# Optimization experiments

Measured on AMD Instinct MI355X. Metric: run time of the kernel, lower is better.

## Reference

```python
import jax, jax.numpy as jnp
import numpy as np

H = 16       # num_attention_heads
HKV = 4      # num_key_value_heads
HD = 128     # head_dim
G = H // HKV # num_key_value_groups


def setup_inputs() -> dict:
    key = jax.random.key(0)
    ks = jax.random.split(key, 7)
    s = 0.02
    B, S, D = 2, 2048, 2048
    return {
        "hidden_states": jax.random.normal(ks[0], (B, S, D), jnp.float32),
        "Wq": jax.random.normal(ks[1], (D, H * HD), jnp.float32) * s,
        "Wk": jax.random.normal(ks[2], (D, HKV * HD), jnp.float32) * s,
        "Wv": jax.random.normal(ks[3], (D, HKV * HD), jnp.float32) * s,
        "Wg": jax.random.normal(ks[4], (H * HD, HKV), jnp.float32) * s,
        "Wd": jax.random.normal(ks[5], (HKV * HD, HKV), jnp.float32) * s,
        "Wo": jax.random.normal(ks[6], (H * HD, D), jnp.float32) * s,
    }


def reference(hidden_states, Wq, Wk, Wv, Wg, Wd, Wo):
    b, s, _ = hidden_states.shape
    scale = HD ** -0.5

    q_flat = hidden_states @ Wq                    # [b,s,H*HD]
    k_flat = hidden_states @ Wk                    # [b,s,HKV*HD]
    v_flat = hidden_states @ Wv                    # [b,s,HKV*HD]

    gate = q_flat @ Wg                             # [b,s,HKV] (per query pos)
    delta = v_flat @ Wd                            # [b,s,HKV] (per key pos)
    # attn_bias: [b,HKV,key_len] after transpose; broadcast over query dim
    bias = (jax.nn.sigmoid(gate) * delta).transpose(0, 2, 1)  # [b,HKV,s]

    # [b,HKV,G,s,HD] query grouped by kv-head; [b,HKV,s,HD] key/value
    q = q_flat.reshape(b, s, HKV, G, HD).transpose(0, 2, 3, 1, 4)
    k = k_flat.reshape(b, s, HKV, HD).transpose(0, 2, 1, 3)
    v = v_flat.reshape(b, s, HKV, HD).transpose(0, 2, 1, 3)

    scores = jnp.einsum('bngqd,bnkd->bngqk', q, k) * scale  # [b,HKV,G,s,s]
    logits = scores + bias[:, :, None, None, :]

    causal = jnp.tril(jnp.ones((s, s), dtype=bool))
    # 'relu' mask: key positions allowed only where relu(bias) > 0
    allowed = causal[None, None, None] & (bias > 0)[:, :, None, None, :]
    neg = jnp.finfo(logits.dtype).min
    logits = jnp.where(allowed, logits, neg)

    p = jax.nn.softmax(logits, axis=-1)
    o = jnp.einsum('bngqk,bnkd->bngqd', p, v)               # [b,HKV,G,s,HD]
    o = o.transpose(0, 3, 1, 2, 4).reshape(b, s, H * HD)
    return o @ Wo
```

## Files before the change

### kernel.cpp

```cpp
#include <hip/hip_runtime.h>
#include <hip/hip_bf16.h>
#include <cmath>
#include <cstdint>

typedef __attribute__((ext_vector_type(8))) short short8;
typedef __attribute__((ext_vector_type(4))) float floatx4;
typedef __attribute__((ext_vector_type(4))) unsigned int uintx4;

typedef const __attribute__((address_space(1))) unsigned int* gas_p;
typedef __attribute__((address_space(3))) unsigned int* las_p;

#define LOG2E 1.4426950408889634f

__device__ inline unsigned short f2bf(float f) {
  unsigned int u = __builtin_bit_cast(unsigned int, f);
  unsigned int r = (u + 0x7FFFu + ((u >> 16) & 1u)) >> 16;
  return (unsigned short)r;
}
__device__ inline float bf2f(unsigned short h) {
  unsigned int u = ((unsigned int)h) << 16;
  return __builtin_bit_cast(float, u);
}

__global__ void k_f32_to_bf16(const float* __restrict__ in, unsigned short* __restrict__ out, int n4) {
  int i = blockIdx.x * 256 + threadIdx.x;
  if (i >= n4) return;
  float4 v = reinterpret_cast<const float4*>(in)[i];
  uint2 o;
  o.x = (unsigned)f2bf(v.x) | ((unsigned)f2bf(v.y) << 16);
  o.y = (unsigned)f2bf(v.z) | ((unsigned)f2bf(v.w) << 16);
  reinterpret_cast<uint2*>(out)[i] = o;
}

__global__ void k_transpose_w(const float* __restrict__ in, unsigned short* __restrict__ out,
                              int K, int N, float scl) {
  __shared__ float t[32][33];
  int n0 = blockIdx.x * 32, k0 = blockIdx.y * 32;
  int tx = threadIdx.x & 31, ty = threadIdx.x >> 5;
  #pragma unroll
  for (int r = ty; r < 32; r += 8)
    t[r][tx] = in[(long)(k0 + r) * N + n0 + tx];
  __syncthreads();
  #pragma unroll
  for (int r = ty; r < 32; r += 8)
    out[(long)(n0 + r) * K + k0 + tx] = f2bf(t[tx][r] * scl);
}

__global__ void k_wproj(const float* __restrict__ W, const float* __restrict__ Ws,
                        float* __restrict__ out, int Kw) {
  int d = blockIdx.x;
  float a0 = 0, a1 = 0, a2 = 0, a3 = 0;
  for (int j = threadIdx.x; j < Kw; j += 256) {
    float w = W[(long)d * Kw + j];
    float4 g = reinterpret_cast<const float4*>(Ws)[j];
    a0 += w * g.x; a1 += w * g.y; a2 += w * g.z; a3 += w * g.w;
  }
  #pragma unroll
  for (int off = 1; off < 64; off <<= 1) {
    a0 += __shfl_xor(a0, off, 64); a1 += __shfl_xor(a1, off, 64);
    a2 += __shfl_xor(a2, off, 64); a3 += __shfl_xor(a3, off, 64);
  }
  __shared__ float red[4][4];
  if ((threadIdx.x & 63) == 0) {
    int wv = threadIdx.x >> 6;
    red[wv][0] = a0; red[wv][1] = a1; red[wv][2] = a2; red[wv][3] = a3;
  }
  __syncthreads();
  if (threadIdx.x < 4) {
    int nn = threadIdx.x;
    out[d * 4 + nn] = red[0][nn] + red[1][nn] + red[2][nn] + red[3][nn];
  }
}

__global__ void k_bias(const float* __restrict__ hs, const float* __restrict__ Wqg,
                       const float* __restrict__ Wvd, float* __restrict__ bias) {
  int row = blockIdx.x;
  int b = row >> 11, s = row & 2047;
  float g0 = 0, g1 = 0, g2 = 0, g3 = 0, d0 = 0, d1 = 0, d2 = 0, d3 = 0;
  const float* h = hs + (long)row * 2048;
  for (int j = threadIdx.x; j < 2048; j += 256) {
    float x = h[j];
    float4 a = reinterpret_cast<const float4*>(Wqg)[j];
    float4 c = reinterpret_cast<const float4*>(Wvd)[j];
    g0 += x * a.x; g1 += x * a.y; g2 += x * a.z; g3 += x * a.w;
    d0 += x * c.x; d1 += x * c.y; d2 += x * c.z; d3 += x * c.w;
  }
  #pragma unroll
  for (int off = 1; off < 64; off <<= 1) {
    g0 += __shfl_xor(g0, off, 64); g1 += __shfl_xor(g1, off, 64);
    g2 += __shfl_xor(g2, off, 64); g3 += __shfl_xor(g3, off, 64);
    d0 += __shfl_xor(d0, off, 64); d1 += __shfl_xor(d1, off, 64);
    d2 += __shfl_xor(d2, off, 64); d3 += __shfl_xor(d3, off, 64);
  }
  __shared__ float red[4][8];
  if ((threadIdx.x & 63) == 0) {
    int wv = threadIdx.x >> 6;
    red[wv][0] = g0; red[wv][1] = g1; red[wv][2] = g2; red[wv][3] = g3;
    red[wv][4] = d0; red[wv][5] = d1; red[wv][6] = d2; red[wv][7] = d3;
  }
  __syncthreads();
  if (threadIdx.x < 4) {
    int nn = threadIdx.x;
    float gg = red[0][nn] + red[1][nn] + red[2][nn] + red[3][nn];
    float dd = red[0][4 + nn] + red[1][4 + nn] + red[2][4 + nn] + red[3][4 + nn];
    float sig = 1.0f / (1.0f + __expf(-gg));
    float v = sig * dd;
    bias[(b * 4 + nn) * 2048 + s] = (v > 0.0f) ? v * LOG2E : -INFINITY;
  }
}

template <int WRITE_BF16>
__global__ __launch_bounds__(256, 2) void k_gemm_bt(
    const unsigned short* __restrict__ A, const unsigned short* __restrict__ Bt,
    void* __restrict__ Cout, int M, int N, int K) {
  __shared__ __align__(16) unsigned short As[128 * 32];
  __shared__ __align__(16) unsigned short Bs[128 * 32];
  const int tid = threadIdx.x;
  const int lane = tid & 63, wave = tid >> 6;
  const int quad = lane >> 4, l16 = lane & 15;
  const long bm = (long)blockIdx.y * 128, bn = (long)blockIdx.x * 128;
  const int wm = (wave >> 1) * 64, wn = (wave & 1) * 64;

  const floatx4 fz = {0.f, 0.f, 0.f, 0.f};
  floatx4 acc[4][4];
  #pragma unroll
  for (int i = 0; i < 4; i++)
    #pragma unroll
    for (int j = 0; j < 4; j++) acc[i][j] = fz;

  const int r0 = tid >> 2, c0 = (tid & 3) * 8;
  const unsigned short* Ag = A + (bm + r0) * K + c0;
  const unsigned short* Bg = Bt + (bn + r0) * K + c0;
  unsigned short* AsW0 = As + (wave * 16) * 32;
  unsigned short* AsW1 = As + (wave * 16 + 64) * 32;
  unsigned short* BsW0 = Bs + (wave * 16) * 32;
  unsigned short* BsW1 = Bs + (wave * 16 + 64) * 32;

  for (int kt = 0; kt < K; kt += 32) {
    __syncthreads();
    __builtin_amdgcn_global_load_lds((gas_p)(const void*)(Ag + kt),
                                     (las_p)(void*)AsW0, 16, 0, 0);
    __builtin_amdgcn_global_load_lds((gas_p)(const void*)(Ag + (long)64 * K + kt),
                                     (las_p)(void*)AsW1, 16, 0, 0);
    __builtin_amdgcn_global_load_lds((gas_p)(const void*)(Bg + kt),
                                     (las_p)(void*)BsW0, 16, 0, 0);
    __builtin_amdgcn_global_load_lds((gas_p)(const void*)(Bg + (long)64 * K + kt),
                                     (las_p)(void*)BsW1, 16, 0, 0);
    __syncthreads();
    short8 af[4], bf[4];
    #pragma unroll
    for (int i = 0; i < 4; i++)
      af[i] = *reinterpret_cast<const short8*>(&As[(wm + i * 16 + l16) * 32 + quad * 8]);
    #pragma unroll
    for (int j = 0; j < 4; j++)
      bf[j] = *reinterpret_cast<const short8*>(&Bs[(wn + j * 16 + l16) * 32 + quad * 8]);
    #pragma unroll
    for (int i = 0; i < 4; i++)
      #pragma unroll
      for (int j = 0; j < 4; j++)
        acc[i][j] = __builtin_amdgcn_mfma_f32_16x16x32_bf16(af[i], bf[j], acc[i][j], 0, 0, 0);
  }
  #pragma unroll
  for (int i = 0; i < 4; i++)
    #pragma unroll
    for (int j = 0; j < 4; j++)
      #pragma unroll
      for (int r = 0; r < 4; r++) {
        const long row = bm + wm + i * 16 + quad * 4 + r;
        const long col = bn + wn + j * 16 + l16;
        const float v = acc[i][j][r];
        if (WRITE_BF16)
          ((unsigned short*)Cout)[row * N + col] = f2bf(v);
        else
          ((float*)Cout)[row * N + col] = v;
      }
}

__global__ void k_transpose_v(const unsigned short* __restrict__ qkv, unsigned short* __restrict__ vt) {
  __shared__ unsigned short t[32][33];
  int c0 = blockIdx.x * 32, s0 = blockIdx.y * 32, b = blockIdx.z;
  int tx = threadIdx.x & 31, ty = threadIdx.x >> 5;
  #pragma unroll
  for (int r = ty; r < 32; r += 8)
    t[r][tx] = qkv[((long)(b * 2048 + s0 + r)) * 3072 + 2560 + c0 + tx];
  __syncthreads();
  #pragma unroll
  for (int r = ty; r < 32; r += 8)
    vt[((long)(b * 512 + c0 + r)) * 2048 + s0 + tx] = t[tx][r];
}

__global__ void k_vmean2(const unsigned short* __restrict__ vT, float* __restrict__ vmean) {
  const int row = blockIdx.x;
  const int tid = threadIdx.x, lane = tid & 63, wave = tid >> 6;
  uintx4 v = reinterpret_cast<const uintx4*>(vT + (long)row * 2048)[tid];
  float s = 0.f;
  #pragma unroll
  for (int i = 0; i < 4; i++) {
    unsigned u = v[i];
    s += bf2f((unsigned short)(u & 0xffff)) + bf2f((unsigned short)(u >> 16));
  }
  #pragma unroll
  for (int off = 1; off < 64; off <<= 1) s += __shfl_xor(s, off, 64);
  __shared__ float red[4];
  if (lane == 0) red[wave] = s;
  __syncthreads();
  if (tid == 0) vmean[row] = (red[0] + red[1] + red[2] + red[3]) * (1.0f / 2048.0f);
}

__global__ __launch_bounds__(256, 3) void k_attn(
    const unsigned short* __restrict__ qkv,
    const float* __restrict__ biasb,
    const unsigned short* __restrict__ vT,
    const float* __restrict__ vmean,
    unsigned short* __restrict__ o)
{
  int idx = blockIdx.x;
  const int g = idx & 3;
  const int n = (idx >> 2) & 3;
  const int b = (idx >> 4) & 1;
  const int qt = 31 - (idx >> 5);
  const int tid = threadIdx.x, lane = tid & 63, wave = tid >> 6;
  const int quad = lane >> 4, l16 = lane & 15;
  const int q0 = qt * 64 + wave * 16;

  __shared__ __align__(16) unsigned short Ks[64 * 144];
  __shared__ __align__(16) unsigned short Vs[128 * 72];
  __shared__ __align__(16) unsigned short Ps[4 * 16 * 72];
  unsigned short* Psw = Ps + wave * 1152;

  short8 qf[4];
  {
    const unsigned short* qp = qkv + (long)(b * 2048) * 3072 + (n * 4 + g) * 128;
    #pragma unroll
    for (int ks = 0; ks < 4; ks++)
      qf[ks] = *reinterpret_cast<const short8*>(
          qp + (long)(q0 + l16) * 3072 + ks * 32 + quad * 8);
  }

  const floatx4 fz = {0.f, 0.f, 0.f, 0.f};
  floatx4 oacc[8];
  #pragma unroll
  for (int j = 0; j < 8; j++) oacc[j] = fz;
  float mrow = -INFINITY, lrow = 0.0f;

  const float* biasrow = biasb + (b * 4 + n) * 2048;
  const unsigned short* kbase = qkv + (long)(b * 2048) * 3072 + 2048 + n * 128;
  const unsigned short* vbase = vT + (long)(b * 512 + n * 128) * 2048;
  const int kk_ = tid >> 4, hdo_ = (tid & 15) * 8;
  const int hd_ = tid >> 3, ko_ = (tid & 7) * 8;

  uintx4 kreg[4], vreg[4];
  float4 breg[4];
  {
    const unsigned short* kp = kbase;
    const unsigned short* vp = vbase;
    #pragma unroll
    for (int it = 0; it < 4; it++)
      kreg[it] = *reinterpret_cast<const uintx4*>(kp + (long)(kk_ + it * 16) * 3072 + hdo_);
    #pragma unroll
    for (int it = 0; it < 4; it++)
      vreg[it] = *reinterpret_cast<const uintx4*>(vp + (long)(hd_ + it * 32) * 2048 + ko_);
    #pragma unroll
    for (int kt = 0; kt < 4; kt++)
      breg[kt] = *reinterpret_cast<const float4*>(biasrow + kt * 16 + quad * 4);
  }

  const int kend = qt * 64 + 64;
  for (int k0 = 0; k0 < kend; k0 += 64) {
    __syncthreads();
    #pragma unroll
    for (int it = 0; it < 4; it++)
      *reinterpret_cast<uintx4*>(&Ks[(kk_ + it * 16) * 144 + hdo_]) = kreg[it];
    #pragma unroll
    for (int it = 0; it < 4; it++)
      *reinterpret_cast<uintx4*>(&Vs[(hd_ + it * 32) * 72 + ko_]) = vreg[it];
    float4 bcur[4];
    #pragma unroll
    for (int kt = 0; kt < 4; kt++) bcur[kt] = breg[kt];

    if (k0 + 64 < kend) {
      const unsigned short* kp = kbase + (long)(k0 + 64) * 3072;
      const unsigned short* vp = vbase + (k0 + 64);
      #pragma unroll
      for (int it = 0; it < 4; it++)
        kreg[it] = *reinterpret_cast<const uintx4*>(kp + (long)(kk_ + it * 16) * 3072 + hdo_);
      #pragma unroll
      for (int it = 0; it < 4; it++)
        vreg[it] = *reinterpret_cast<const uintx4*>(vp + (long)(hd_ + it * 32) * 2048 + ko_);
      #pragma unroll
      for (int kt = 0; kt < 4; kt++)
        breg[kt] = *reinterpret_cast<const float4*>(biasrow + (k0 + 64) + kt * 16 + quad * 4);
    }
    __syncthreads();

    const bool active = (k0 <= q0 + 15);
    if (active) {
      floatx4 sacc[4];
      #pragma unroll
      for (int kt = 0; kt < 4; kt++)
        sacc[kt] = (floatx4){bcur[kt].x, bcur[kt].y, bcur[kt].z, bcur[kt].w};
      #pragma unroll
      for (int ks = 0; ks < 4; ks++) {
        short8 kf[4];
        #pragma unroll
        for (int kt = 0; kt < 4; kt++)
          kf[kt] = *reinterpret_cast<const short8*>(&Ks[(kt * 16 + l16) * 144 + ks * 32 + quad * 8]);
        #pragma unroll
        for (int kt = 0; kt < 4; kt++)
          sacc[kt] = __builtin_amdgcn_mfma_f32_16x16x32_bf16(kf[kt], qf[ks], sacc[kt], 0, 0, 0);
      }

      const bool full = (k0 + 63 <= q0);
      if (!full) {
        const int diff = (q0 + l16) - (k0 + quad * 4);
        #pragma unroll
        for (int kt = 0; kt < 4; kt++)
          #pragma unroll
          for (int r = 0; r < 4; r++)
            if (kt * 16 + r > diff) sacc[kt][r] = -INFINITY;
      }
      float mx = -INFINITY;
      #pragma unroll
      for (int kt = 0; kt < 4; kt++)
        #pragma unroll
        for (int r = 0; r < 4; r++) mx = fmaxf(mx, sacc[kt][r]);
      mx = fmaxf(mx, __shfl_xor(mx, 16, 64));
      mx = fmaxf(mx, __shfl_xor(mx, 32, 64));
      const float mn = fmaxf(mrow, mx);
      const float mnc = fmaxf(mn, -1e38f);
      const float alpha = __builtin_amdgcn_exp2f(mrow - mnc);
      float rs = 0.0f;
      unsigned pk[4][2];
      #pragma unroll
      for (int kt = 0; kt < 4; kt++) {
        #pragma unroll
        for (int r = 0; r < 4; r++) {
          float p = __builtin_amdgcn_exp2f(sacc[kt][r] - mnc);
          sacc[kt][r] = p;
          rs += p;
        }
        #pragma unroll
        for (int r2 = 0; r2 < 2; r2++)
          pk[kt][r2] = (unsigned)f2bf(sacc[kt][2 * r2]) | ((unsigned)f2bf(sacc[kt][2 * r2 + 1]) << 16);
      }
      rs += __shfl_xor(rs, 16, 64);
      rs += __shfl_xor(rs, 32, 64);
      mrow = mn;
      lrow = lrow * alpha + rs;

      float al[4];
      #pragma unroll
      for (int r = 0; r < 4; r++) al[r] = __shfl(alpha, quad * 4 + r, 64);
      #pragma unroll
      for (int j = 0; j < 8; j++)
        #pragma unroll
        for (int r = 0; r < 4; r++) oacc[j][r] *= al[r];

      unsigned* Pd = reinterpret_cast<unsigned*>(Psw);
      #pragma unroll
      for (int kt = 0; kt < 4; kt++)
        #pragma unroll
        for (int r2 = 0; r2 < 2; r2++)
          Pd[l16 * 36 + kt * 8 + quad * 2 + r2] = pk[kt][r2];

      #pragma unroll
      for (int ks2 = 0; ks2 < 2; ks2++) {
        short8 pf = *reinterpret_cast<const short8*>(&Psw[l16 * 72 + ks2 * 32 + quad * 8]);
        #pragma unroll
        for (int j = 0; j < 8; j++) {
          short8 vf = *reinterpret_cast<const short8*>(&Vs[(j * 16 + l16) * 72 + ks2 * 32 + quad * 8]);
          oacc[j] = __builtin_amdgcn_mfma_f32_16x16x32_bf16(pf, vf, oacc[j], 0, 0, 0);
        }
      }
    }
  }

  const long obase = (long)(b * 2048) * 2048 + (n * 4 + g) * 128;
  #pragma unroll
  for (int r = 0; r < 4; r++) {
    const int qrow = q0 + quad * 4 + r;
    const float l = __shfl(lrow, quad * 4 + r, 64);
    const float inv = (l > 0.0f) ? 1.0f / l : 0.0f;
    #pragma unroll
    for (int j = 0; j < 8; j++) {
      const int hd = j * 16 + l16;
      float v = oacc[j][r] * inv;
      if (l <= 0.0f) v = vmean[(b * 4 + n) * 128 + hd];
      o[obase + (long)qrow * 2048 + hd] = f2bf(v);
    }
  }
}

extern "C" void kernel_launch(void* const* d_in, const int* in_sizes, int n_in,
                              void* d_out, int out_size, void* d_ws, size_t ws_size,
                              hipStream_t stream) {
  const float* hs = (const float*)d_in[0];
  const float* Wq = (const float*)d_in[1];
  const float* Wk = (const float*)d_in[2];
  const float* Wv = (const float*)d_in[3];
  const float* Wg = (const float*)d_in[4];
  const float* Wd = (const float*)d_in[5];
  const float* Wo = (const float*)d_in[6];
  float* out = (float*)d_out;

  char* ws = (char*)d_ws;
  unsigned short* hsb   = (unsigned short*)(ws);
  unsigned short* Wcomb = (unsigned short*)(ws + 16777216);
  unsigned short* Wot   = (unsigned short*)(ws + 29360128);
  float*  Wqg   = (float*)(ws + 37748736);
  float*  Wvd   = (float*)(ws + 37781504);
  float*  biasb = (float*)(ws + 37814272);
  unsigned short* qkv = (unsigned short*)(ws + 37879808);
  unsigned short* vT  = (unsigned short*)(ws + 63045632);
  float*  vmean = (float*)(ws + 67239936);
  unsigned short* ob  = (unsigned short*)(ws + 67244032);

  const float QSCALE = 0.08838834764831845f * LOG2E;

  k_f32_to_bf16<<<2097152 / 256, 256, 0, stream>>>(hs, hsb, 2097152);

  {
    dim3 g1(2048 / 32, 2048 / 32);
    dim3 g2(512 / 32, 2048 / 32);
    k_transpose_w<<<g1, 256, 0, stream>>>(Wq, Wcomb, 2048, 2048, QSCALE);
    k_transpose_w<<<g2, 256, 0, stream>>>(Wk, Wcomb + (long)2048 * 2048, 2048, 512, 1.0f);
    k_transpose_w<<<g2, 256, 0, stream>>>(Wv, Wcomb + (long)2560 * 2048, 2048, 512, 1.0f);
    k_transpose_w<<<g1, 256, 0, stream>>>(Wo, Wot, 2048, 2048, 1.0f);
  }

  k_wproj<<<2048, 256, 0, stream>>>(Wq, Wg, Wqg, 2048);
  k_wproj<<<2048, 256, 0, stream>>>(Wv, Wd, Wvd, 512);

  k_bias<<<4096, 256, 0, stream>>>(hs, Wqg, Wvd, biasb);

  {
    dim3 gq(3072 / 128, 4096 / 128);
    k_gemm_bt<1><<<gq, 256, 0, stream>>>(hsb, Wcomb, qkv, 4096, 3072, 2048);
  }

  {
    dim3 gv(16, 64, 2);
    k_transpose_v<<<gv, 256, 0, stream>>>(qkv, vT);
  }

  k_vmean2<<<1024, 256, 0, stream>>>(vT, vmean);

  k_attn<<<1024, 256, 0, stream>>>(qkv, biasb, vT, vmean, ob);

  {
    dim3 go(2048 / 128, 4096 / 128);
    k_gemm_bt<0><<<go, 256, 0, stream>>>(ob, Wot, out, 4096, 2048, 2048);
  }
}
```

Before: 348.4 us.

## Swizzle LDS tiles, lazy softmax rescale, interleave tile order, raise occupancy

Replaces padded LDS layouts for K, V and P with XOR-swizzled unpadded layouts. This cuts shared memory use and lets launch bounds ask for 4 blocks per CU instead of 3. It reorders query tiles across the grid to balance causal work, and skips the output rescale when the running max grows by no more than 8 (in log2 units). It also adds s_setprio around the MFMA sections and uses the hardware packed bf16 convert instruction. The lazy rescale may risk overflow or precision loss, and the swizzle must match between writes and reads.

```diff
diff --git a/kernel.cpp b/kernel.cpp
--- a/kernel.cpp
+++ b/kernel.cpp
@@ -207,7 +207,7 @@
   if (tid == 0) vmean[row] = (red[0] + red[1] + red[2] + red[3]) * (1.0f / 2048.0f);
 }
 
-__global__ __launch_bounds__(256, 3) void k_attn(
+__global__ __launch_bounds__(256, 4) void k_attn(
     const unsigned short* __restrict__ qkv,
     const float* __restrict__ biasb,
     const unsigned short* __restrict__ vT,
@@ -218,15 +218,22 @@
   const int g = idx & 3;
   const int n = (idx >> 2) & 3;
   const int b = (idx >> 4) & 1;
-  const int qt = 31 - (idx >> 5);
+  const int i5 = idx >> 5, pj = i5 & 7, phi = i5 >> 3;
+  int qt;
+  if (phi == 0) qt = 31 - pj;
+  else if (phi == 1) qt = pj;
+  else if (phi == 2) qt = 23 - pj;
+  else qt = 8 + pj;
+
   const int tid = threadIdx.x, lane = tid & 63, wave = tid >> 6;
   const int quad = lane >> 4, l16 = lane & 15;
   const int q0 = qt * 64 + wave * 16;
 
-  __shared__ __align__(16) unsigned short Ks[64 * 144];
-  __shared__ __align__(16) unsigned short Vs[128 * 72];
-  __shared__ __align__(16) unsigned short Ps[4 * 16 * 72];
-  unsigned short* Psw = Ps + wave * 1152;
+  __shared__ __align__(16) unsigned short Ks[64 * 128];
+  __shared__ __align__(16) unsigned short Vs[128 * 64];
+  __shared__ __align__(16) unsigned short Ps[4 * 16 * 64];
+  unsigned short* Psw = Ps + wave * 1024;
+  const int swz = (l16 & 7) << 3;
 
   short8 qf[4];
   {
@@ -248,6 +255,8 @@
   const unsigned short* vbase = vT + (long)(b * 512 + n * 128) * 2048;
   const int kk_ = tid >> 4, hdo_ = (tid & 15) * 8;
   const int hd_ = tid >> 3, ko_ = (tid & 7) * 8;
+  const int kswz = (kk_ & 7) << 3;
+  const int vswz = (hd_ & 7) << 3;
 
   uintx4 kreg[4], vreg[4];
   float4 breg[4];
@@ -270,10 +279,10 @@
     __syncthreads();
     #pragma unroll
     for (int it = 0; it < 4; it++)
-      *reinterpret_cast<uintx4*>(&Ks[(kk_ + it * 16) * 144 + hdo_]) = kreg[it];
+      *reinterpret_cast<uintx4*>(&Ks[(kk_ + it * 16) * 128 + (hdo_ ^ kswz)]) = kreg[it];
     #pragma unroll
     for (int it = 0; it < 4; it++)
-      *reinterpret_cast<uintx4*>(&Vs[(hd_ + it * 32) * 72 + ko_]) = vreg[it];
+      *reinterpret_cast<uintx4*>(&Vs[(hd_ + it * 32) * 64 + (ko_ ^ vswz)]) = vreg[it];
     float4 bcur[4];
     #pragma unroll
     for (int kt = 0; kt < 4; kt++) bcur[kt] = breg[kt];
@@ -299,16 +308,19 @@
       #pragma unroll
       for (int kt = 0; kt < 4; kt++)
         sacc[kt] = (floatx4){bcur[kt].x, bcur[kt].y, bcur[kt].z, bcur[kt].w};
+      __builtin_amdgcn_s_setprio(1);
       #pragma unroll
       for (int ks = 0; ks < 4; ks++) {
         short8 kf[4];
         #pragma unroll
         for (int kt = 0; kt < 4; kt++)
-          kf[kt] = *reinterpret_cast<const short8*>(&Ks[(kt * 16 + l16) * 144 + ks * 32 + quad * 8]);
+          kf[kt] = *reinterpret_cast<const short8*>(
+              &Ks[(kt * 16 + l16) * 128 + ((ks * 32 + quad * 8) ^ swz)]);
         #pragma unroll
         for (int kt = 0; kt < 4; kt++)
           sacc[kt] = __builtin_amdgcn_mfma_f32_16x16x32_bf16(kf[kt], qf[ks], sacc[kt], 0, 0, 0);
       }
+      __builtin_amdgcn_s_setprio(0);
 
       const bool full = (k0 + 63 <= q0);
       if (!full) {
@@ -326,9 +338,21 @@
         for (int r = 0; r < 4; r++) mx = fmaxf(mx, sacc[kt][r]);
       mx = fmaxf(mx, __shfl_xor(mx, 16, 64));
       mx = fmaxf(mx, __shfl_xor(mx, 32, 64));
-      const float mn = fmaxf(mrow, mx);
-      const float mnc = fmaxf(mn, -1e38f);
-      const float alpha = __builtin_amdgcn_exp2f(mrow - mnc);
+      if (!__all(mx <= mrow + 8.0f)) {
+        const float mn = fmaxf(mrow, mx);
+        const float mnc2 = fmaxf(mn, -1e38f);
+        const float alpha = __builtin_amdgcn_exp2f(mrow - mnc2);
+        float al[4];
+        #pragma unroll
+        for (int r = 0; r < 4; r++) al[r] = __shfl(alpha, quad * 4 + r, 64);
+        #pragma unroll
+        for (int j = 0; j < 8; j++)
+          #pragma unroll
+          for (int r = 0; r < 4; r++) oacc[j][r] *= al[r];
+        lrow *= alpha;
+        mrow = mn;
+      }
+      const float mnc = fmaxf(mrow, -1e38f);
       float rs = 0.0f;
       unsigned pk[4][2];
       #pragma unroll
@@ -339,39 +363,35 @@
           sacc[kt][r] = p;
           rs += p;
         }
-        #pragma unroll
-        for (int r2 = 0; r2 < 2; r2++)
-          pk[kt][r2] = (unsigned)f2bf(sacc[kt][2 * r2]) | ((unsigned)f2bf(sacc[kt][2 * r2 + 1]) << 16);
+        {
+          float s0 = sacc[kt][0], s1 = sacc[kt][1], s2 = sacc[kt][2], s3 = sacc[kt][3];
+          asm("v_cvt_pk_bf16_f32 %0, %1, %2" : "=v"(pk[kt][0]) : "v"(s0), "v"(s1));
+          asm("v_cvt_pk_bf16_f32 %0, %1, %2" : "=v"(pk[kt][1]) : "v"(s2), "v"(s3));
+        }
       }
       rs += __shfl_xor(rs, 16, 64);
       rs += __shfl_xor(rs, 32, 64);
-      mrow = mn;
-      lrow = lrow * alpha + rs;
-
-      float al[4];
-      #pragma unroll
-      for (int r = 0; r < 4; r++) al[r] = __shfl(alpha, quad * 4 + r, 64);
-      #pragma unroll
-      for (int j = 0; j < 8; j++)
-        #pragma unroll
-        for (int r = 0; r < 4; r++) oacc[j][r] *= al[r];
-
-      unsigned* Pd = reinterpret_cast<unsigned*>(Psw);
-      #pragma unroll
-      for (int kt = 0; kt < 4; kt++)
-        #pragma unroll
-        for (int r2 = 0; r2 < 2; r2++)
-          Pd[l16 * 36 + kt * 8 + quad * 2 + r2] = pk[kt][r2];
-
+      lrow += rs;
+
+      #pragma unroll
+      for (int kt = 0; kt < 4; kt++) {
+        uint2 u; u.x = pk[kt][0]; u.y = pk[kt][1];
+        *reinterpret_cast<uint2*>(&Psw[l16 * 64 + ((kt * 16 + quad * 4) ^ swz)]) = u;
+      }
+
+      __builtin_amdgcn_s_setprio(1);
       #pragma unroll
       for (int ks2 = 0; ks2 < 2; ks2++) {
-        short8 pf = *reinterpret_cast<const short8*>(&Psw[l16 * 72 + ks2 * 32 + quad * 8]);
+        short8 pf = *reinterpret_cast<const short8*>(
+            &Psw[l16 * 64 + ((ks2 * 32 + quad * 8) ^ swz)]);
         #pragma unroll
         for (int j = 0; j < 8; j++) {
-          short8 vf = *reinterpret_cast<const short8*>(&Vs[(j * 16 + l16) * 72 + ks2 * 32 + quad * 8]);
+          short8 vf = *reinterpret_cast<const short8*>(
+              &Vs[(j * 16 + l16) * 64 + ((ks2 * 32 + quad * 8) ^ swz)]);
           oacc[j] = __builtin_amdgcn_mfma_f32_16x16x32_bf16(pf, vf, oacc[j], 0, 0, 0);
         }
       }
+      __builtin_amdgcn_s_setprio(0);
     }
   }
 
```

New measurement: 591.5 us. 1.7x slower.
